# Optimization experiments

Hardware: AMD Instinct MI355X
Metric: run time of the kernel (lower is better)

## Reference

```python
import jax, jax.numpy as jnp
import numpy as np

N_QUBITS = 8
N_PAIRS = 4
PAIRS = [(2 * p, 2 * p + 1) for p in range(N_PAIRS)]
STRENGTH = 0.8
DIM = 2 ** N_QUBITS


def _apply_1q_full(st, G, q):
    # st: (2,)*n complex64 state, G: [2,2] gate on qubit q (qubit 0 = most significant)
    out = jnp.tensordot(G, st, axes=([1], [q]))
    return jnp.moveaxis(out, 0, q)


def _apply_ctrl_full(st, G, c, t):
    # controlled-G: apply G on target axis t only where control axis c == 1
    s0 = jnp.take(st, 0, axis=c)
    s1 = jnp.take(st, 1, axis=c)
    t2 = t if t < c else t - 1
    s1 = jnp.moveaxis(jnp.tensordot(G, s1, axes=([1], [t2])), 0, t2)
    return jnp.stack([s0, s1], axis=c)


def _entangled_base():
    # |0...0> -> H on q1, partial CNOT (controlled-RX(pi*strength)) on (q1,q2) per pair
    st = jnp.zeros((2,) * N_QUBITS, jnp.complex64).at[(0,) * N_QUBITS].set(1.0)
    H = jnp.array([[1.0, 1.0], [1.0, -1.0]], jnp.complex64) / np.float32(np.sqrt(2.0))
    th = np.float32(np.pi * STRENGTH)
    c, s = np.float32(np.cos(th / 2)), np.float32(np.sin(th / 2))
    RX = jnp.array([[c, -1j * s], [-1j * s, c]], jnp.complex64)
    for q1, q2 in PAIRS:
        st = _apply_1q_full(st, H, q1)
        st = _apply_ctrl_full(st, RX, q1, q2)
    return st.reshape(-1)


def _rx(theta):
    # RX(theta) = [[cos t/2, -i sin t/2], [-i sin t/2, cos t/2]], batched over theta shape
    cz = jnp.cos(0.5 * theta).astype(jnp.complex64)
    sz = (-1j) * jnp.sin(0.5 * theta).astype(jnp.complex64)
    return jnp.stack([jnp.stack([cz, sz], -1), jnpp_stack_fix(sz, cz)], -2) if False else jnp.stack([jnp.stack([cz, sz], -1), jnp.stack([sz, cz], -1)], -2)


def _rz(theta):
    ph = (0.5j) * theta.astype(jnp.complex64)
    e0, e1 = jnp.exp(-ph), jnp.exp(ph)
    z = jnp.zeros_like(e0)
    return jnp.stack([jnp.stack([e0, z], -1), jnp.stack([z, e1], -1)], -2)


def _quantum_scores(k_states):
    # k_states: [B,S,2*n_qubits] -> expected pair-agreement score [B,S]
    B, S, _ = k_states.shape
    k = k_states.reshape(B, S, N_QUBITS, 2)
    eye = jnp.eye(2, dtype=jnp.complex64)
    st = jnp.broadcast_to(_entangled_base(), (B, S, DIM))  # fresh entangled register per (b,j)
    for q in range(N_QUBITS):
        th_x, th_z = k[:, :, q, 0], k[:, :, q, 1]
        Gx = jnp.where((th_x > 0)[..., None, None], _rx(th_x), eye)
        Gz = jnp.where((th_z > 0)[..., None, None], _rz(th_z), eye)
        G = jnp.einsum('bsij,bsjk->bsik', Gz, Gx)  # RX applied first, then RZ
        L = 2 ** q
        R = DIM // (2 * L)
        stv = st.reshape(B, S, L, 2, R)
        st = jnp.einsum('bsij,bsljr->bslir', G, stv).reshape(B, S, DIM)
    probs = (st.real ** 2 + st.imag ** 2).reshape((B, S) + (2,) * N_QUBITS)
    score = jnp.zeros((B, S), probs.dtype)
    for q1, q2 in PAIRS:
        axes = tuple(2 + a for a in range(N_QUBITS) if a not in (q1, q2))
        marg = probs.sum(axis=axes)  # [B,S,2,2] joint marginal of the pair
        score = score + marg[..., 0, 0] + marg[..., 1, 1]  # P(measure equal)
    return score / N_PAIRS


def reference(query, key, value, Wq, bq, Wk, bk, Wv, bv, Wo, bo):
    q_states = query @ Wq + bq  # computed as in original forward (unused by scores)
    k_states = key @ Wk + bk    # [B,S,2*n_qubits]
    v_states = value @ Wv + bv  # [B,S,d_model]
    B, S, _ = k_states.shape
    score = _quantum_scores(k_states)  # [B,S]; deterministic expected agreement
    # original loop makes score[b,i,j] independent of i under independent per-(b,i,j) sims
    attn = jnp.broadcast_to(score[:, None, :], (B, S, S))
    w = jax.nn.softmax(attn, axis=-1)
    out = jnp.einsum('bij,bjd->bid', w, v_states)
    return out @ Wo + bo


def setup_inputs() -> dict:
    rng = jax.random.key(0)
    ks = jax.random.split(rng, 8)
    B, S, D = 8, 2048, 512
    nq2 = 2 * N_QUBITS
    f = jax.random.normal
    return {
        'query': f(ks[0], (B, S, D), jnp.float32),
        'key': f(ks[1], (B, S, D), jnp.float32),
        'value': f(ks[2], (B, S, D), jnp.float32),
        'Wq': f(ks[3], (D, nq2), jnp.float32) * 0.05,
        'bq': jnp.zeros((nq2,), jnp.float32),
        'Wk': f(ks[4], (D, nq2), jnp.float32) * 0.05,
        'bk': jnp.zeros((nq2,), jnp.float32),
        'Wv': f(ks[5], (D, D), jnp.float32) * 0.05,
        'bv': jnp.zeros((D,), jnp.float32),
        'Wo': f(ks[6], (D, D), jnp.float32) * 0.05,
        'bo': jnp.zeros((D,), jnp.float32),
    }
```

## Files before the change

### kernel.cpp

```cpp
#include <hip/hip_runtime.h>
#include <math.h>

#define DEV __device__ __forceinline__

struct C2 { float x, y; };
DEV C2 cmul(C2 a, C2 b){ return {a.x*b.x - a.y*b.y, a.x*b.y + a.y*b.x}; }
DEV C2 cadd(C2 a, C2 b){ return {a.x+b.x, a.y+b.y}; }
DEV C2 cscale(C2 a, float s){ return {a.x*s, a.y*s}; }
DEV C2 cnegi(C2 a){ return {a.y, -a.x}; }

__global__ __launch_bounds__(512, 2) void k_score_wsum(const float* __restrict__ key,
                                                       const float* __restrict__ Wk,
                                                       const float* __restrict__ bk,
                                                       const float* __restrict__ value,
                                                       float* __restrict__ partial,
                                                       float* __restrict__ partialw)
{
    const int c = blockIdx.x;
    const int b = blockIdx.y;
    const int t = threadIdx.x;
    const int lane = t & 63;
    const int wv   = t >> 6;
    const int h    = wv & 1;
    const int pr   = wv >> 1;
    const int base = b * 2048 + c * 32;
    const int wrow0 = pr * 8;

    __shared__ float  kslds[2][32][16];
    __shared__ float4 red[8][128];
    __shared__ float  wsums[4];

    const float4* kp = (const float4*)(key + (size_t)(base + wrow0) * 512);
    float4 krow[8];
    #pragma unroll
    for (int j = 0; j < 8; ++j) krow[j] = kp[j * 128 + h * 64 + lane];

    float4 wk[4][4];
    #pragma unroll
    for (int jj = 0; jj < 4; ++jj) {
        const float4* w0 = (const float4*)(Wk + (h * 256 + 4 * lane + jj) * 16);
        #pragma unroll
        for (int q = 0; q < 4; ++q) wk[jj][q] = w0[q];
    }

    const int vrow0 = wrow0 + h * 4;
    const float4* vp = (const float4*)(value + (size_t)(base + vrow0) * 512);
    float4 vreg[8];
    #pragma unroll
    for (int j = 0; j < 4; ++j) {
        vreg[2*j]   = vp[j * 128 + lane];
        vreg[2*j+1] = vp[j * 128 + 64 + lane];
    }

    const float c0 = 0.30901699437494745f;
    const float s0 = 0.9510565162951535f;

    #pragma unroll
    for (int j = 0; j < 8; ++j) {
        float el[4] = {krow[j].x, krow[j].y, krow[j].z, krow[j].w};
        float acc[16];
        #pragma unroll
        for (int k = 0; k < 16; ++k) acc[k] = 0.f;
        #pragma unroll
        for (int jj = 0; jj < 4; ++jj) {
            #pragma unroll
            for (int q = 0; q < 4; ++q) {
                acc[4*q+0] = fmaf(el[jj], wk[jj][q].x, acc[4*q+0]);
                acc[4*q+1] = fmaf(el[jj], wk[jj][q].y, acc[4*q+1]);
                acc[4*q+2] = fmaf(el[jj], wk[jj][q].z, acc[4*q+2]);
                acc[4*q+3] = fmaf(el[jj], wk[jj][q].w, acc[4*q+3]);
            }
        }
        #pragma unroll
        for (int s = 0; s < 4; ++s) {
            const int m = 1 << s;
            const int bbit = (lane >> s) & 1;
            #pragma unroll
            for (int jj = 0; jj < (16 >> (s + 1)); ++jj) {
                float send = bbit ? acc[2*jj] : acc[2*jj+1];
                float keep = bbit ? acc[2*jj+1] : acc[2*jj];
                acc[jj] = keep + __shfl_xor(send, m);
            }
        }
        float ks = acc[0];
        ks += __shfl_xor(ks, 16);
        ks += __shfl_xor(ks, 32);
        if (lane < 16) kslds[h][wrow0 + j][lane] = ks;
    }
    __syncthreads();

    const int p  = (lane >> 3) & 3;
    const int jr = lane & 7;
    float4 k0 = *(const float4*)&kslds[0][wrow0 + jr][4 * p];
    float4 k1 = *(const float4*)&kslds[1][wrow0 + jr][4 * p];
    float4 bk4 = ((const float4*)bk)[p];
    float ax = k0.x + k1.x + bk4.x, az = k0.y + k1.y + bk4.y;
    float bx = k0.z + k1.z + bk4.z, bz = k0.w + k1.w + bk4.w;
    float cxa = 1.f, sxa = 0.f; if (ax > 0.f){ sxa = __sinf(0.5f*ax); cxa = __cosf(0.5f*ax); }
    float cpa = 1.f, spa = 0.f; if (az > 0.f){ spa = __sinf(0.5f*az); cpa = __cosf(0.5f*az); }
    float cxb = 1.f, sxb = 0.f; if (bx > 0.f){ sxb = __sinf(0.5f*bx); cxb = __cosf(0.5f*bx); }
    float cpb = 1.f, spb = 0.f; if (bz > 0.f){ spb = __sinf(0.5f*bz); cpb = __cosf(0.5f*bz); }
    C2 A00{cpa*cxa, -spa*cxa}, A01{-spa*sxa, -cpa*sxa};
    C2 A10{spa*sxa, -cpa*sxa}, A11{ cpa*cxa,  spa*cxa};
    C2 B00{cpb*cxb, -spb*cxb}, B01{-spb*sxb, -cpb*sxb};
    C2 B10{spb*sxb, -cpb*sxb}, B11{ cpb*cxb,  spb*cxb};
    C2 u = cadd(cmul(B00, cadd(A00, cscale(A01, c0))),
                cscale(cnegi(cmul(A01, B01)), s0));
    C2 v = cadd(cmul(B10, cadd(A10, cscale(A11, c0))),
                cscale(cnegi(cmul(A11, B11)), s0));
    float ps = u.x*u.x + u.y*u.y + v.x*v.x + v.y*v.y;
    ps += __shfl_xor(ps, 8);
    ps += __shfl_xor(ps, 16);
    float w_all = __expf(ps * 0.125f);

    if (h == 0) {
        float sw = w_all;
        sw += __shfl_xor(sw, 1); sw += __shfl_xor(sw, 2); sw += __shfl_xor(sw, 4);
        if (lane == 0) wsums[pr] = sw;
    }

    float4 aA = {0.f,0.f,0.f,0.f}, aB = {0.f,0.f,0.f,0.f};
    #pragma unroll
    for (int j = 0; j < 4; ++j) {
        float wj = __shfl(w_all, h * 4 + j);
        float4 v0 = vreg[2*j], v1 = vreg[2*j+1];
        aA.x = fmaf(wj, v0.x, aA.x); aA.y = fmaf(wj, v0.y, aA.y);
        aA.z = fmaf(wj, v0.z, aA.z); aA.w = fmaf(wj, v0.w, aA.w);
        aB.x = fmaf(wj, v1.x, aB.x); aB.y = fmaf(wj, v1.y, aB.y);
        aB.z = fmaf(wj, v1.z, aB.z); aB.w = fmaf(wj, v1.w, aB.w);
    }
    red[wv][lane] = aA;
    red[wv][64 + lane] = aB;
    __syncthreads();
    if (t < 128) {
        float4 q0 = red[0][t], q1 = red[1][t], q2 = red[2][t], q3 = red[3][t];
        float4 q4 = red[4][t], q5 = red[5][t], q6 = red[6][t], q7 = red[7][t];
        float4 o = { q0.x+q1.x+q2.x+q3.x+q4.x+q5.x+q6.x+q7.x,
                     q0.y+q1.y+q2.y+q3.y+q4.y+q5.y+q6.y+q7.y,
                     q0.z+q1.z+q2.z+q3.z+q4.z+q5.z+q6.z+q7.z,
                     q0.w+q1.w+q2.w+q3.w+q4.w+q5.w+q6.w+q7.w };
        ((float4*)partial)[((size_t)b * 64 + c) * 128 + t] = o;
    }
    if (t == 0)
        partialw[b * 64 + c] = wsums[0] + wsums[1] + wsums[2] + wsums[3];
}

__global__ __launch_bounds__(512) void k_mid(const float* __restrict__ partial,
                                             const float* __restrict__ partialw,
                                             const float* __restrict__ Wv,
                                             const float* __restrict__ bv,
                                             const float* __restrict__ Wo,
                                             const float* __restrict__ bo,
                                             float* __restrict__ frow)
{
    const int dt = blockIdx.x;
    const int b  = blockIdx.y;
    const int t  = threadIdx.x;

    __shared__ float cbuf[512];
    __shared__ float xbuf[512];
    __shared__ float red[512];
    __shared__ float sS;

    if (t < 64) {
        float s = partialw[b * 64 + t];
        s += __shfl_xor(s, 1);  s += __shfl_xor(s, 2);
        s += __shfl_xor(s, 4);  s += __shfl_xor(s, 8);
        s += __shfl_xor(s, 16); s += __shfl_xor(s, 32);
        if (t == 0) sS = 1.f / s;
    }

    {
        float c0 = 0.f, c1 = 0.f, c2 = 0.f, c3 = 0.f;
        const float* pp = partial + (size_t)b * 32768 + t;
        #pragma unroll
        for (int cc = 0; cc < 64; cc += 4) {
            c0 += pp[(size_t)cc * 512];
            c1 += pp[(size_t)(cc + 1) * 512];
            c2 += pp[(size_t)(cc + 2) * 512];
            c3 += pp[(size_t)(cc + 3) * 512];
        }
        cbuf[t] = (c0 + c1) + (c2 + c3);
    }
    __syncthreads();
    const float invS = sS;

    {
        float a0=0.f,a1=0.f,a2=0.f,a3=0.f,a4=0.f,a5=0.f,a6=0.f,a7=0.f;
        #pragma unroll 8
        for (int e = 0; e < 512; e += 8) {
            a0 = fmaf(cbuf[e],   Wv[(size_t)e * 512 + t],     a0);
            a1 = fmaf(cbuf[e+1], Wv[(size_t)(e+1) * 512 + t], a1);
            a2 = fmaf(cbuf[e+2], Wv[(size_t)(e+2) * 512 + t], a2);
            a3 = fmaf(cbuf[e+3], Wv[(size_t)(e+3) * 512 + t], a3);
            a4 = fmaf(cbuf[e+4], Wv[(size_t)(e+4) * 512 + t], a4);
            a5 = fmaf(cbuf[e+5], Wv[(size_t)(e+5) * 512 + t], a5);
            a6 = fmaf(cbuf[e+6], Wv[(size_t)(e+6) * 512 + t], a6);
            a7 = fmaf(cbuf[e+7], Wv[(size_t)(e+7) * 512 + t], a7);
        }
        xbuf[t] = (((a0+a1)+(a2+a3)) + ((a4+a5)+(a6+a7))) * invS + bv[t];
    }
    __syncthreads();

    {
        const int dl = t & 63, g = t >> 6;
        const int d  = dt * 64 + dl;
        const float* Wc = Wo + (size_t)(g * 64) * 512 + d;
        const float* xg = xbuf + g * 64;
        float a0=0.f,a1=0.f,a2=0.f,a3=0.f;
        #pragma unroll 8
        for (int e = 0; e < 64; e += 4) {
            a0 = fmaf(xg[e],   Wc[(size_t)e * 512],       a0);
            a1 = fmaf(xg[e+1], Wc[(size_t)(e+1) * 512],   a1);
            a2 = fmaf(xg[e+2], Wc[(size_t)(e+2) * 512],   a2);
            a3 = fmaf(xg[e+3], Wc[(size_t)(e+3) * 512],   a3);
        }
        red[t] = (a0 + a1) + (a2 + a3);
    }
    __syncthreads();
    if (t < 64) {
        float r = red[t]       + red[t + 64]  + red[t + 128] + red[t + 192]
                + red[t + 256] + red[t + 320] + red[t + 384] + red[t + 448];
        frow[b * 512 + dt * 64 + t] = r + bo[dt * 64 + t];
    }
}

__global__ __launch_bounds__(256) void k_bcast(const float* __restrict__ frow,
                                               float* __restrict__ out)
{
    int s = blockIdx.x, b = blockIdx.y, t = threadIdx.x;
    const int col4 = t & 127, h = t >> 7;
    float4 val = ((const float4*)frow)[b * 128 + col4];
    float4* o4 = (float4*)out
               + ((size_t)b * 2048 + s * 32 + h * 16) * 128 + col4;
    #pragma unroll
    for (int r = 0; r < 16; ++r) o4[(size_t)r * 128] = val;
}

extern "C" void kernel_launch(void* const* d_in, const int* in_sizes, int n_in,
                              void* d_out, int out_size, void* d_ws, size_t ws_size,
                              hipStream_t stream) {
    const float* key   = (const float*)d_in[1];
    const float* value = (const float*)d_in[2];
    const float* Wk    = (const float*)d_in[5];
    const float* bk    = (const float*)d_in[6];
    const float* Wv    = (const float*)d_in[7];
    const float* bv    = (const float*)d_in[8];
    const float* Wo    = (const float*)d_in[9];
    const float* bo    = (const float*)d_in[10];
    float* out = (float*)d_out;
    float* ws  = (float*)d_ws;

    float* partial  = ws;
    float* partialw = ws + 262144;
    float* frow     = ws + 262656;

    k_score_wsum<<<dim3(64, 8), 512, 0, stream>>>(key, Wk, bk, value,
                                                  partial, partialw);
    k_mid       <<<dim3(8, 8),  512, 0, stream>>>(partial, partialw,
                                                  Wv, bv, Wo, bo, frow);
    k_bcast     <<<dim3(64, 8), 256, 0, stream>>>(frow, out);
}
```

Before: 170.8 us.

## Compute key projection via LDS-transposed Wk with per-thread row-column dot products

Replaces the register-resident Wk slice plus butterfly shuffle reduction with staging Wk transposed in shared memory. Each thread then computes one full 512-long dot product for one (row, output column) pair. Each wave now owns 4 rows directly, which changes the score and weight-sum reductions. This removes the many cross-lane shuffles, but each thread now reads a whole key row with strided, uncoalesced float4 loads, and the block must first stage Wk, adding an extra barrier and about 33KB of LDS. The launch_bounds occupancy hint of 2 blocks per SM is also dropped.

```diff
diff --git a/kernel.cpp b/kernel.cpp
--- a/kernel.cpp
+++ b/kernel.cpp
@@ -9,42 +9,26 @@
 DEV C2 cscale(C2 a, float s){ return {a.x*s, a.y*s}; }
 DEV C2 cnegi(C2 a){ return {a.y, -a.x}; }
 
-__global__ __launch_bounds__(512, 2) void k_score_wsum(const float* __restrict__ key,
-                                                       const float* __restrict__ Wk,
-                                                       const float* __restrict__ bk,
-                                                       const float* __restrict__ value,
-                                                       float* __restrict__ partial,
-                                                       float* __restrict__ partialw)
+__global__ __launch_bounds__(512) void k_score_wsum(const float* __restrict__ key,
+                                                    const float* __restrict__ Wk,
+                                                    const float* __restrict__ bk,
+                                                    const float* __restrict__ value,
+                                                    float* __restrict__ partial,
+                                                    float* __restrict__ partialw)
 {
     const int c = blockIdx.x;
     const int b = blockIdx.y;
     const int t = threadIdx.x;
     const int lane = t & 63;
     const int wv   = t >> 6;
-    const int h    = wv & 1;
-    const int pr   = wv >> 1;
     const int base = b * 2048 + c * 32;
-    const int wrow0 = pr * 8;
-
-    __shared__ float  kslds[2][32][16];
+
+    __shared__ float  wkT[16][524];
+    __shared__ float  kslds[32][20];
     __shared__ float4 red[8][128];
-    __shared__ float  wsums[4];
-
-    const float4* kp = (const float4*)(key + (size_t)(base + wrow0) * 512);
-    float4 krow[8];
-    #pragma unroll
-    for (int j = 0; j < 8; ++j) krow[j] = kp[j * 128 + h * 64 + lane];
-
-    float4 wk[4][4];
-    #pragma unroll
-    for (int jj = 0; jj < 4; ++jj) {
-        const float4* w0 = (const float4*)(Wk + (h * 256 + 4 * lane + jj) * 16);
-        #pragma unroll
-        for (int q = 0; q < 4; ++q) wk[jj][q] = w0[q];
-    }
-
-    const int vrow0 = wrow0 + h * 4;
-    const float4* vp = (const float4*)(value + (size_t)(base + vrow0) * 512);
+    __shared__ float  wsums[8];
+
+    const float4* vp = (const float4*)(value + (size_t)(base + wv * 4) * 512);
     float4 vreg[8];
     #pragma unroll
     for (int j = 0; j < 4; ++j) {
@@ -52,50 +36,56 @@
         vreg[2*j+1] = vp[j * 128 + 64 + lane];
     }
 
+    {
+        const float4* wk4 = (const float4*)Wk;
+        #pragma unroll
+        for (int k = 0; k < 4; ++k) {
+            int l = t + k * 512;
+            float4 w = wk4[l];
+            int e = l >> 2, c4 = (l & 3) * 4;
+            wkT[c4 + 0][e] = w.x;
+            wkT[c4 + 1][e] = w.y;
+            wkT[c4 + 2][e] = w.z;
+            wkT[c4 + 3][e] = w.w;
+        }
+    }
+    __syncthreads();
+
+    {
+        const int row = t >> 4, col = t & 15;
+        const float4* kp = (const float4*)(key + (size_t)(base + row) * 512);
+        const float4* wt = (const float4*)&wkT[col][0];
+        float a0=0.f,a1=0.f,a2=0.f,a3=0.f,a4=0.f,a5=0.f,a6=0.f,a7=0.f;
+        #pragma unroll
+        for (int e4 = 0; e4 < 128; e4 += 8) {
+            float4 k0 = kp[e4+0], w0 = wt[e4+0];
+            float4 k1 = kp[e4+1], w1 = wt[e4+1];
+            float4 k2 = kp[e4+2], w2 = wt[e4+2];
+            float4 k3 = kp[e4+3], w3 = wt[e4+3];
+            float4 k4 = kp[e4+4], w4 = wt[e4+4];
+            float4 k5 = kp[e4+5], w5 = wt[e4+5];
+            float4 k6 = kp[e4+6], w6 = wt[e4+6];
+            float4 k7 = kp[e4+7], w7 = wt[e4+7];
+            a0 = fmaf(k0.x,w0.x, fmaf(k0.y,w0.y, fmaf(k0.z,w0.z, fmaf(k0.w,w0.w, a0))));
+            a1 = fmaf(k1.x,w1.x, fmaf(k1.y,w1.y, fmaf(k1.z,w1.z, fmaf(k1.w,w1.w, a1))));
+            a2 = fmaf(k2.x,w2.x, fmaf(k2.y,w2.y, fmaf(k2.z,w2.z, fmaf(k2.w,w2.w, a2))));
+            a3 = fmaf(k3.x,w3.x, fmaf(k3.y,w3.y, fmaf(k3.z,w3.z, fmaf(k3.w,w3.w, a3))));
+            a4 = fmaf(k4.x,w4.x, fmaf(k4.y,w4.y, fmaf(k4.z,w4.z, fmaf(k4.w,w4.w, a4))));
+            a5 = fmaf(k5.x,w5.x, fmaf(k5.y,w5.y, fmaf(k5.z,w5.z, fmaf(k5.w,w5.w, a5))));
+            a6 = fmaf(k6.x,w6.x, fmaf(k6.y,w6.y, fmaf(k6.z,w6.z, fmaf(k6.w,w6.w, a6))));
+            a7 = fmaf(k7.x,w7.x, fmaf(k7.y,w7.y, fmaf(k7.z,w7.z, fmaf(k7.w,w7.w, a7))));
+        }
+        float ks = (((a0+a1)+(a2+a3)) + ((a4+a5)+(a6+a7))) + bk[col];
+        kslds[row][col] = ks;
+    }
+    __syncthreads();
+
     const float c0 = 0.30901699437494745f;
     const float s0 = 0.9510565162951535f;
-
-    #pragma unroll
-    for (int j = 0; j < 8; ++j) {
-        float el[4] = {krow[j].x, krow[j].y, krow[j].z, krow[j].w};
-        float acc[16];
-        #pragma unroll
-        for (int k = 0; k < 16; ++k) acc[k] = 0.f;
-        #pragma unroll
-        for (int jj = 0; jj < 4; ++jj) {
-            #pragma unroll
-            for (int q = 0; q < 4; ++q) {
-                acc[4*q+0] = fmaf(el[jj], wk[jj][q].x, acc[4*q+0]);
-                acc[4*q+1] = fmaf(el[jj], wk[jj][q].y, acc[4*q+1]);
-                acc[4*q+2] = fmaf(el[jj], wk[jj][q].z, acc[4*q+2]);
-                acc[4*q+3] = fmaf(el[jj], wk[jj][q].w, acc[4*q+3]);
-            }
-        }
-        #pragma unroll
-        for (int s = 0; s < 4; ++s) {
-            const int m = 1 << s;
-            const int bbit = (lane >> s) & 1;
-            #pragma unroll
-            for (int jj = 0; jj < (16 >> (s + 1)); ++jj) {
-                float send = bbit ? acc[2*jj] : acc[2*jj+1];
-                float keep = bbit ? acc[2*jj+1] : acc[2*jj];
-                acc[jj] = keep + __shfl_xor(send, m);
-            }
-        }
-        float ks = acc[0];
-        ks += __shfl_xor(ks, 16);
-        ks += __shfl_xor(ks, 32);
-        if (lane < 16) kslds[h][wrow0 + j][lane] = ks;
-    }
-    __syncthreads();
-
-    const int p  = (lane >> 3) & 3;
-    const int jr = lane & 7;
-    float4 k0 = *(const float4*)&kslds[0][wrow0 + jr][4 * p];
-    float4 k1 = *(const float4*)&kslds[1][wrow0 + jr][4 * p];
-    float4 bk4 = ((const float4*)bk)[p];
-    float ax = k0.x + k1.x + bk4.x, az = k0.y + k1.y + bk4.y;
-    float bx = k0.z + k1.z + bk4.z, bz = k0.w + k1.w + bk4.w;
+    const int p  = (lane >> 2) & 3;
+    const int jr = lane & 3;
+    const float* kr = &kslds[wv * 4 + jr][4 * p];
+    float ax = kr[0], az = kr[1], bx = kr[2], bz = kr[3];
     float cxa = 1.f, sxa = 0.f; if (ax > 0.f){ sxa = __sinf(0.5f*ax); cxa = __cosf(0.5f*ax); }
     float cpa = 1.f, spa = 0.f; if (az > 0.f){ spa = __sinf(0.5f*az); cpa = __cosf(0.5f*az); }
     float cxb = 1.f, sxb = 0.f; if (bx > 0.f){ sxb = __sinf(0.5f*bx); cxb = __cosf(0.5f*bx); }
@@ -109,20 +99,20 @@
     C2 v = cadd(cmul(B10, cadd(A10, cscale(A11, c0))),
                 cscale(cnegi(cmul(A11, B11)), s0));
     float ps = u.x*u.x + u.y*u.y + v.x*v.x + v.y*v.y;
+    ps += __shfl_xor(ps, 4);
     ps += __shfl_xor(ps, 8);
-    ps += __shfl_xor(ps, 16);
     float w_all = __expf(ps * 0.125f);
 
-    if (h == 0) {
+    {
         float sw = w_all;
-        sw += __shfl_xor(sw, 1); sw += __shfl_xor(sw, 2); sw += __shfl_xor(sw, 4);
-        if (lane == 0) wsums[pr] = sw;
+        sw += __shfl_xor(sw, 1); sw += __shfl_xor(sw, 2);
+        if (lane == 0) wsums[wv] = sw;
     }
 
     float4 aA = {0.f,0.f,0.f,0.f}, aB = {0.f,0.f,0.f,0.f};
     #pragma unroll
     for (int j = 0; j < 4; ++j) {
-        float wj = __shfl(w_all, h * 4 + j);
+        float wj = __shfl(w_all, j);
         float4 v0 = vreg[2*j], v1 = vreg[2*j+1];
         aA.x = fmaf(wj, v0.x, aA.x); aA.y = fmaf(wj, v0.y, aA.y);
         aA.z = fmaf(wj, v0.z, aA.z); aA.w = fmaf(wj, v0.w, aA.w);
@@ -142,7 +132,8 @@
         ((float4*)partial)[((size_t)b * 64 + c) * 128 + t] = o;
     }
     if (t == 0)
-        partialw[b * 64 + c] = wsums[0] + wsums[1] + wsums[2] + wsums[3];
+        partialw[b * 64 + c] = wsums[0] + wsums[1] + wsums[2] + wsums[3]
+                             + wsums[4] + wsums[5] + wsums[6] + wsums[7];
 }
 
 __global__ __launch_bounds__(512) void k_mid(const float* __restrict__ partial,
```

After: 177.1 us. +3.7%, slower.
